# Kernel tuning notes

Measured on AMD Instinct MI355X. Metric: run time of the kernel, lower is better.

## Reference

```python
import jax, jax.numpy as jnp
import numpy as np

CUTOFF = 10.0
CUTOFF_SR = 4.0
KEHALF = 7.199822675975274
OFFSET2 = 1.0
N_ATOMS = 100000
N_EDGES = 3200000


def switch_fn(d):
    # smooth poly5 switch: 1 at d=0, 0 at d>=cutoff_short_range
    x = d / CUTOFF_SR
    s = 1.0 - x * x * x * (10.0 - 15.0 * x + 6.0 * x * x)
    return jnp.where(x < 1.0, s, 0.0)


def setup_inputs() -> dict:
    key = jax.random.key(0)
    k1, k2, k3, k4, k5, k6 = jax.random.split(key, 6)
    atomic_charges = jax.random.normal(k1, (N_ATOMS,), dtype=jnp.float32)
    atomic_dipoles = jax.random.normal(k2, (N_ATOMS, 3), dtype=jnp.float32)
    atomic_quadrupoles = jax.random.normal(k3, (N_ATOMS, 3, 3), dtype=jnp.float32)
    vectors_uv = 3.0 * jax.random.normal(k4, (N_EDGES, 3), dtype=jnp.float32)
    distances_uv = jnp.linalg.norm(vectors_uv, axis=-1)  # consistent, >0, some > cutoff
    idx_u = jax.random.randint(k5, (N_EDGES,), 0, N_ATOMS, dtype=jnp.int32)
    idx_v = jax.random.randint(k6, (N_EDGES,), 0, N_ATOMS, dtype=jnp.int32)
    return {
        'atomic_charges': atomic_charges,
        'atomic_dipoles': atomic_dipoles,
        'atomic_quadrupoles': atomic_quadrupoles,
        'vectors_uv': vectors_uv,
        'distances_uv': distances_uv,
        'idx_u': idx_u,
        'idx_v': idx_v,
    }


def reference(atomic_charges, atomic_dipoles, atomic_quadrupoles,
              vectors_uv, distances_uv, idx_u, idx_v):
    d = distances_uv                                  # [E]
    d_damped = jnp.sqrt(d * d + OFFSET2)
    sw = switch_fn(d)
    chi = sw / d_damped + (1.0 - sw) / d
    cutoff2 = CUTOFF * CUTOFF
    chi_shift = 2.0 / CUTOFF - d / cutoff2

    q_u = atomic_charges[idx_u]                       # [E]
    q_v = atomic_charges[idx_v]
    Eelec = q_u * q_v * (chi - chi_shift)

    chi2 = chi * chi
    chi3 = chi2 * chi
    cutoff3 = cutoff2 * CUTOFF
    cutoff4 = cutoff3 * CUTOFF
    chi2_shift = 3.0 / cutoff2 - 2.0 * d / cutoff3
    chi3_shift = 4.0 / cutoff3 - 3.0 * d / cutoff4

    # dipole contributions
    nvec = vectors_uv / d[:, None]                    # [E,3] normalized
    dip_u = atomic_dipoles[idx_u]
    dip_v = atomic_dipoles[idx_v]
    dot_uv = jnp.sum(nvec * dip_v, axis=1)
    dot_vu = jnp.sum(nvec * dip_u, axis=1)
    Eelec_cd = 2.0 * q_u * dot_uv * (chi2 - chi2_shift)
    Eelec_dd = (jnp.sum(dip_u * dip_v, axis=1) - 3.0 * dot_uv * dot_vu) * (chi3 - chi3_shift)
    Eelec = Eelec + Eelec_cd + Eelec_dd

    # quadrupole contributions
    outer = vectors_uv[:, :, None] * vectors_uv[:, None, :]      # [E,3,3]
    trace_mean = jnp.trace(outer, axis1=-2, axis2=-1) / 3.0      # [E]
    traceless = outer - trace_mean[:, None, None] * jnp.eye(3, dtype=outer.dtype)
    traceless = traceless / (d * d)[:, None, None]
    quad_v = atomic_quadrupoles[idx_v]                           # [E,3,3]
    sum_uv = jnp.sum(traceless * quad_v, axis=(1, 2))
    Eelec = Eelec + q_u * sum_uv * (chi3 - chi3_shift)

    Eelec = KEHALF * Eelec
    return jnp.where(d <= CUTOFF, Eelec, jnp.zeros_like(Eelec))
```

## Files before the change

kernel.cpp:

```cpp
#include <hip/hip_runtime.h>


#define CUTOFF      10.0f
#define KEHALF      7.199822675975274f

typedef float    f32x4 __attribute__((ext_vector_type(4)));
typedef unsigned u32x4 __attribute__((ext_vector_type(4)));

__device__ __forceinline__ unsigned f2bf(float f) {
    unsigned u = __float_as_uint(f);
    return (u + 0x7FFFu + ((u >> 16) & 1u)) >> 16;
}
__device__ __forceinline__ float bflo(unsigned p) { return __uint_as_float(p << 16); }
__device__ __forceinline__ float bfhi(unsigned p) { return __uint_as_float(p & 0xFFFF0000u); }

__global__ __launch_bounds__(256) void pack_atoms_kernel(
    const float* __restrict__ q,
    const float* __restrict__ dip,
    const float* __restrict__ quad,
    f32x4* __restrict__ table,
    int N)
{
    int i = blockIdx.x * blockDim.x + threadIdx.x;
    if (i >= N) return;
    const float* dp = dip + 3 * (size_t)i;
    const float* qp = quad + 9 * (size_t)i;

    f32x4 w0 = {q[i], dp[0], dp[1], dp[2]};

    float q00 = qp[0], q01 = qp[1], q02 = qp[2];
    float q10 = qp[3], q11 = qp[4], q12 = qp[5];
    float q20 = qp[6], q21 = qp[7], q22 = qp[8];
    float trQ3 = (q00 + q11 + q22) * (1.0f / 3.0f);

    unsigned p0 = f2bf(q00 - trQ3) | (f2bf(q11 - trQ3) << 16);
    unsigned p1 = f2bf(q22 - trQ3) | (f2bf(q01 + q10) << 16);
    unsigned p2 = f2bf(q02 + q20) | (f2bf(q12 + q21) << 16);
    u32x4 w1 = {p0, p1, p2, 0u};

    table[2 * (size_t)i + 0] = w0;
    table[2 * (size_t)i + 1] = __builtin_bit_cast(f32x4, w1);
}

__device__ __forceinline__ float edge_energy(
    float vx, float vy, float vz,
    f32x4 au, f32x4 av, u32x4 bv)
{
    float d2 = vx * vx + vy * vy + vz * vz;
    float d = sqrtf(d2);
    float inv_d = 1.0f / d;
    float inv_d2 = inv_d * inv_d;

    float x = d * 0.25f;
    float x2 = x * x;
    float x3 = x2 * x;
    float sw = 1.0f - x3 * (10.0f - 15.0f * x + 6.0f * x2);
    sw = (x < 1.0f) ? sw : 0.0f;
    float chi = sw * rsqrtf(d2 + 1.0f) + (1.0f - sw) * inv_d;

    float c1 = chi - (0.2f   - 0.01f   * d);
    float chi2 = chi * chi;
    float chi3 = chi2 * chi;
    float c2 = chi2 - (0.03f  - 0.002f  * d);
    float c3 = chi3 - (0.004f - 0.0003f * d);

    float qu = au.x, qv = av.x;
    float Ee = qu * qv * c1;

    float dot_uv = (vx * av.y + vy * av.z + vz * av.w) * inv_d;
    float dot_vu = (vx * au.y + vy * au.z + vz * au.w) * inv_d;
    float dd     = au.y * av.y + au.z * av.z + au.w * av.w;

    Ee += 2.0f * qu * dot_uv * c2;
    Ee += (dd - 3.0f * dot_uv * dot_vu) * c3;

    float t00 = bflo(bv.x), t11 = bfhi(bv.x);
    float t22 = bflo(bv.y), s01 = bfhi(bv.y);
    float s02 = bflo(bv.z), s12 = bfhi(bv.z);
    float num = t00 * vx * vx + t11 * vy * vy + t22 * vz * vz
              + s01 * vx * vy + s02 * vx * vz + s12 * vy * vz;
    Ee += qu * (num * inv_d2) * c3;

    Ee *= KEHALF;
    return (d <= CUTOFF) ? Ee : 0.0f;
}

__global__ __launch_bounds__(256) void damped_elec_packed32(
    const f32x4* __restrict__ table,
    const float* __restrict__ vec,
    const int*   __restrict__ idx_u,
    const int*   __restrict__ idx_v,
    float*       __restrict__ out,
    int E)
{
    int i = blockIdx.x * blockDim.x + threadIdx.x;
    if (i >= E) return;

    int u = __builtin_nontemporal_load(idx_u + i);
    int v = __builtin_nontemporal_load(idx_v + i);
    float vx = __builtin_nontemporal_load(vec + 3 * (size_t)i + 0);
    float vy = __builtin_nontemporal_load(vec + 3 * (size_t)i + 1);
    float vz = __builtin_nontemporal_load(vec + 3 * (size_t)i + 2);

    f32x4 au = table[2 * (size_t)u];
    f32x4 av = table[2 * (size_t)v + 0];
    u32x4 bv = __builtin_bit_cast(u32x4, table[2 * (size_t)v + 1]);

    float r = edge_energy(vx, vy, vz, au, av, bv);
    __builtin_nontemporal_store(r, out + i);
}

__global__ __launch_bounds__(256) void damped_elec_unpacked(
    const float* __restrict__ q,
    const float* __restrict__ dip,
    const float* __restrict__ quad,
    const float* __restrict__ vec,
    const int*   __restrict__ idx_u,
    const int*   __restrict__ idx_v,
    float*       __restrict__ out,
    int E)
{
    int i = blockIdx.x * blockDim.x + threadIdx.x;
    if (i >= E) return;
    float vx = vec[3 * (size_t)i + 0];
    float vy = vec[3 * (size_t)i + 1];
    float vz = vec[3 * (size_t)i + 2];
    int u = idx_u[i];
    int v = idx_v[i];
    const float* pu = dip + 3 * (size_t)u;
    const float* pv = dip + 3 * (size_t)v;
    const float* pq = quad + 9 * (size_t)v;

    f32x4 au = {q[u], pu[0], pu[1], pu[2]};
    f32x4 av = {q[v], pv[0], pv[1], pv[2]};
    float trQ3 = (pq[0] + pq[4] + pq[8]) * (1.0f / 3.0f);
    unsigned p0 = f2bf(pq[0] - trQ3) | (f2bf(pq[4] - trQ3) << 16);
    unsigned p1 = f2bf(pq[8] - trQ3) | (f2bf(pq[1] + pq[3]) << 16);
    unsigned p2 = f2bf(pq[2] + pq[6]) | (f2bf(pq[5] + pq[7]) << 16);
    u32x4 bv = {p0, p1, p2, 0u};
    out[i] = edge_energy(vx, vy, vz, au, av, bv);
}

extern "C" void kernel_launch(void* const* d_in, const int* in_sizes, int n_in,
                              void* d_out, int out_size, void* d_ws, size_t ws_size,
                              hipStream_t stream) {
    const float* q    = (const float*)d_in[0];
    const float* dip  = (const float*)d_in[1];
    const float* quad = (const float*)d_in[2];
    const float* vec  = (const float*)d_in[3];
    const int*   iu   = (const int*)d_in[5];
    const int*   iv   = (const int*)d_in[6];
    float* out = (float*)d_out;

    int N = in_sizes[0];
    int E = in_sizes[4];
    int block = 256;
    int egrid = (E + block - 1) / block;

    size_t need = (size_t)N * 32;
    if (ws_size >= need) {
        f32x4* table = (f32x4*)d_ws;
        int pgrid = (N + block - 1) / block;
        pack_atoms_kernel<<<pgrid, block, 0, stream>>>(q, dip, quad, table, N);
        damped_elec_packed32<<<egrid, block, 0, stream>>>(table, vec, iu, iv, out, E);
    } else {
        damped_elec_unpacked<<<egrid, block, 0, stream>>>(q, dip, quad, vec, iu, iv, out, E);
    }
}
```

Measured before the change: 58.26 us.

## Process four edges per thread with vector loads; store quadrupole in fp16

The edge kernel now handles four edges per thread, using 128-bit loads for indices and edge vectors and a 128-bit store for outputs. It also issues all twelve gathers before any compute to raise memory-level parallelism. Separately, the packed traceless quadrupole moves from bf16 to fp16 using hardware conversion instructions, which is cheaper to decode and more precise, but values outside the fp16 range would overflow. The grid shrinks by four, so fewer waves are available to hide latency, and per-thread register use rises.

```diff
diff --git a/kernel.cpp b/kernel.cpp
--- a/kernel.cpp
+++ b/kernel.cpp
@@ -1,18 +1,20 @@
 #include <hip/hip_runtime.h>
+#include <hip/hip_fp16.h>
 
 
 #define CUTOFF      10.0f
 #define KEHALF      7.199822675975274f
 
 typedef float    f32x4 __attribute__((ext_vector_type(4)));
+typedef int      i32x4 __attribute__((ext_vector_type(4)));
 typedef unsigned u32x4 __attribute__((ext_vector_type(4)));
 
-__device__ __forceinline__ unsigned f2bf(float f) {
-    unsigned u = __float_as_uint(f);
-    return (u + 0x7FFFu + ((u >> 16) & 1u)) >> 16;
-}
-__device__ __forceinline__ float bflo(unsigned p) { return __uint_as_float(p << 16); }
-__device__ __forceinline__ float bfhi(unsigned p) { return __uint_as_float(p & 0xFFFF0000u); }
+__device__ __forceinline__ unsigned pack_h2(float a, float b) {
+    return __builtin_bit_cast(unsigned, __floats2half2_rn(a, b));
+}
+__device__ __forceinline__ float2 unpack_h2(unsigned u) {
+    return __half22float2(__builtin_bit_cast(__half2, u));
+}
 
 __global__ __launch_bounds__(256) void pack_atoms_kernel(
     const float* __restrict__ q,
@@ -33,10 +35,10 @@
     float q20 = qp[6], q21 = qp[7], q22 = qp[8];
     float trQ3 = (q00 + q11 + q22) * (1.0f / 3.0f);
 
-    unsigned p0 = f2bf(q00 - trQ3) | (f2bf(q11 - trQ3) << 16);
-    unsigned p1 = f2bf(q22 - trQ3) | (f2bf(q01 + q10) << 16);
-    unsigned p2 = f2bf(q02 + q20) | (f2bf(q12 + q21) << 16);
-    u32x4 w1 = {p0, p1, p2, 0u};
+    u32x4 w1 = {pack_h2(q00 - trQ3, q11 - trQ3),
+                pack_h2(q22 - trQ3, q01 + q10),
+                pack_h2(q02 + q20, q12 + q21),
+                0u};
 
     table[2 * (size_t)i + 0] = w0;
     table[2 * (size_t)i + 1] = __builtin_bit_cast(f32x4, w1);
@@ -74,18 +76,18 @@
     Ee += 2.0f * qu * dot_uv * c2;
     Ee += (dd - 3.0f * dot_uv * dot_vu) * c3;
 
-    float t00 = bflo(bv.x), t11 = bfhi(bv.x);
-    float t22 = bflo(bv.y), s01 = bfhi(bv.y);
-    float s02 = bflo(bv.z), s12 = bfhi(bv.z);
-    float num = t00 * vx * vx + t11 * vy * vy + t22 * vz * vz
-              + s01 * vx * vy + s02 * vx * vz + s12 * vy * vz;
+    float2 h0 = unpack_h2(bv.x);
+    float2 h1 = unpack_h2(bv.y);
+    float2 h2 = unpack_h2(bv.z);
+    float num = h0.x * vx * vx + h0.y * vy * vy + h1.x * vz * vz
+              + h1.y * vx * vy + h2.x * vx * vz + h2.y * vy * vz;
     Ee += qu * (num * inv_d2) * c3;
 
     Ee *= KEHALF;
     return (d <= CUTOFF) ? Ee : 0.0f;
 }
 
-__global__ __launch_bounds__(256) void damped_elec_packed32(
+__global__ __launch_bounds__(256, 4) void damped_elec_4e(
     const f32x4* __restrict__ table,
     const float* __restrict__ vec,
     const int*   __restrict__ idx_u,
@@ -93,21 +95,48 @@
     float*       __restrict__ out,
     int E)
 {
-    int i = blockIdx.x * blockDim.x + threadIdx.x;
-    if (i >= E) return;
-
-    int u = __builtin_nontemporal_load(idx_u + i);
-    int v = __builtin_nontemporal_load(idx_v + i);
-    float vx = __builtin_nontemporal_load(vec + 3 * (size_t)i + 0);
-    float vy = __builtin_nontemporal_load(vec + 3 * (size_t)i + 1);
-    float vz = __builtin_nontemporal_load(vec + 3 * (size_t)i + 2);
-
-    f32x4 au = table[2 * (size_t)u];
-    f32x4 av = table[2 * (size_t)v + 0];
-    u32x4 bv = __builtin_bit_cast(u32x4, table[2 * (size_t)v + 1]);
-
-    float r = edge_energy(vx, vy, vz, au, av, bv);
-    __builtin_nontemporal_store(r, out + i);
+    int t = blockIdx.x * blockDim.x + threadIdx.x;
+    size_t base = 4 * (size_t)t;
+
+    if (base + 3 < (size_t)E) {
+        i32x4 u4 = __builtin_nontemporal_load((const i32x4*)(idx_u + base));
+        i32x4 v4 = __builtin_nontemporal_load((const i32x4*)(idx_v + base));
+        const f32x4* vp = (const f32x4*)(vec + 3 * base);
+        f32x4 w0 = __builtin_nontemporal_load(vp + 0);
+        f32x4 w1 = __builtin_nontemporal_load(vp + 1);
+        f32x4 w2 = __builtin_nontemporal_load(vp + 2);
+
+        int us[4] = {u4.x, u4.y, u4.z, u4.w};
+        int vs[4] = {v4.x, v4.y, v4.z, v4.w};
+
+        f32x4 au[4], av[4], bv[4];
+#pragma unroll
+        for (int e = 0; e < 4; ++e) {
+            au[e] = table[2 * (size_t)us[e]];
+            av[e] = table[2 * (size_t)vs[e] + 0];
+            bv[e] = table[2 * (size_t)vs[e] + 1];
+        }
+
+        float r0 = edge_energy(w0.x, w0.y, w0.z, au[0], av[0], __builtin_bit_cast(u32x4, bv[0]));
+        float r1 = edge_energy(w0.w, w1.x, w1.y, au[1], av[1], __builtin_bit_cast(u32x4, bv[1]));
+        float r2 = edge_energy(w1.z, w1.w, w2.x, au[2], av[2], __builtin_bit_cast(u32x4, bv[2]));
+        float r3 = edge_energy(w2.y, w2.z, w2.w, au[3], av[3], __builtin_bit_cast(u32x4, bv[3]));
+
+        f32x4 res = {r0, r1, r2, r3};
+        __builtin_nontemporal_store(res, (f32x4*)(out + base));
+    } else {
+        for (size_t i = base; i < (size_t)E; ++i) {
+            int u = idx_u[i];
+            int v = idx_v[i];
+            float vx = vec[3 * i + 0];
+            float vy = vec[3 * i + 1];
+            float vz = vec[3 * i + 2];
+            out[i] = edge_energy(vx, vy, vz,
+                                 table[2 * (size_t)u],
+                                 table[2 * (size_t)v],
+                                 __builtin_bit_cast(u32x4, table[2 * (size_t)v + 1]));
+        }
+    }
 }
 
 __global__ __launch_bounds__(256) void damped_elec_unpacked(
@@ -134,10 +163,10 @@
     f32x4 au = {q[u], pu[0], pu[1], pu[2]};
     f32x4 av = {q[v], pv[0], pv[1], pv[2]};
     float trQ3 = (pq[0] + pq[4] + pq[8]) * (1.0f / 3.0f);
-    unsigned p0 = f2bf(pq[0] - trQ3) | (f2bf(pq[4] - trQ3) << 16);
-    unsigned p1 = f2bf(pq[8] - trQ3) | (f2bf(pq[1] + pq[3]) << 16);
-    unsigned p2 = f2bf(pq[2] + pq[6]) | (f2bf(pq[5] + pq[7]) << 16);
-    u32x4 bv = {p0, p1, p2, 0u};
+    u32x4 bv = {pack_h2(pq[0] - trQ3, pq[4] - trQ3),
+                pack_h2(pq[8] - trQ3, pq[1] + pq[3]),
+                pack_h2(pq[2] + pq[6], pq[5] + pq[7]),
+                0u};
     out[i] = edge_energy(vx, vy, vz, au, av, bv);
 }
 
@@ -155,15 +184,17 @@
     int N = in_sizes[0];
     int E = in_sizes[4];
     int block = 256;
-    int egrid = (E + block - 1) / block;
 
     size_t need = (size_t)N * 32;
     if (ws_size >= need) {
         f32x4* table = (f32x4*)d_ws;
         int pgrid = (N + block - 1) / block;
         pack_atoms_kernel<<<pgrid, block, 0, stream>>>(q, dip, quad, table, N);
-        damped_elec_packed32<<<egrid, block, 0, stream>>>(table, vec, iu, iv, out, E);
+        int nthreads = (E + 3) / 4;
+        int egrid = (nthreads + block - 1) / block;
+        damped_elec_4e<<<egrid, block, 0, stream>>>(table, vec, iu, iv, out, E);
     } else {
+        int egrid = (E + block - 1) / block;
         damped_elec_unpacked<<<egrid, block, 0, stream>>>(q, dip, quad, vec, iu, iv, out, E);
     }
 }
```

Measured after the change: 64.17 us. +10.1%, slower.
